# Kernel tuning notes

Measured on AMD Instinct MI355X. Metric: run time of the kernel, lower is better.

Reference implementation:

```python
import jax, jax.numpy as jnp
import numpy as np

B, C, T = 8, 1024, 1024
H, K, R = 8, 8, 8
DQK = C // K      # 128, per-head q/k channels
DFC1 = C // R     # 128, FC hidden
DINNER = C // H   # 128, per-head FC output


def setup_inputs() -> dict:
    key = jax.random.key(0)
    ks = jax.random.split(key, 12)
    s_in = 1.0 / np.sqrt(C)
    s_fc = 1.0 / np.sqrt(DFC1)
    return {
        "x": jax.random.normal(ks[0], (B, C, T), dtype=jnp.float32),
        # per-head 1x1 conv weights stacked over heads
        "Wq": jax.random.normal(ks[1], (H, DQK, C), dtype=jnp.float32) * s_in,
        "bq": jax.random.normal(ks[2], (H, DQK), dtype=jnp.float32) * 0.01,
        "Wk": jax.random.normal(ks[3], (H, DQK, C), dtype=jnp.float32) * s_in,
        "bk": jax.random.normal(ks[4], (H, DQK), dtype=jnp.float32) * 0.01,
        "Wv": jax.random.normal(ks[5], (H, C, C), dtype=jnp.float32) * s_in,
        "bv": jax.random.normal(ks[6], (H, C), dtype=jnp.float32) * 0.01,
        # gamma is zero-init in torch; use small random values to exercise the math
        "gamma": jax.random.normal(ks[7], (H,), dtype=jnp.float32) * 0.1,
        # post-concat MLP (nn.Linear weights, shape (out, in))
        "W1": jax.random.normal(ks[8], (DFC1, C), dtype=jnp.float32) * s_in,
        "b1": jax.random.normal(ks[9], (DFC1,), dtype=jnp.float32) * 0.01,
        "W2": jax.random.normal(ks[10], (DINNER, DFC1), dtype=jnp.float32) * s_fc,
        "b2": jax.random.normal(ks[11], (DINNER,), dtype=jnp.float32) * 0.01,
    }


def reference(x, Wq, bq, Wk, bk, Wv, bv, gamma, W1, b1, W2, b2):
    # x: (B, C, T). 1x1 Conv1d == channel-wise linear; batch all H heads at once.
    q = jnp.einsum('hoc,bct->bhot', Wq, x) + bq[None, :, :, None]  # (B,H,DQK,T)
    k = jnp.einsum('hoc,bct->bhot', Wk, x) + bk[None, :, :, None]  # (B,H,DQK,T)
    v = jnp.einsum('hoc,bct->bhot', Wv, x) + bv[None, :, :, None]  # (B,H,C,T)
    # energy[b,h,t,s] = q[:, :, :, t] . k[:, :, :, s]; softmax over s (no scaling, as in source)
    attn = jax.nn.softmax(jnp.einsum('bhot,bhos->bhts', q, k), axis=-1)  # (B,H,T,T)
    # out[b,h,c,t] = sum_s v[b,h,c,s] * attn[b,h,t,s]
    o = jnp.einsum('bhcs,bhts->bhct', v, attn)                     # (B,H,C,T)
    heads = gamma[None, :, None, None] * o + x[:, None, :, :]      # (B,H,C,T)
    # torch.stack(outs, 2): (B, C, H, T)
    out = heads.transpose(0, 2, 1, 3).reshape(B, C, H * T)
    out = out.transpose(0, 2, 1)                                   # (B, H*T, C)
    # fcs: Linear -> ReLU -> Dropout(eval: identity) -> Linear -> ReLU -> Dropout
    out = jax.nn.relu(out @ W1.T + b1)
    out = jax.nn.relu(out @ W2.T + b2)                             # (B, H*T, DINNER)
    out = out.transpose(0, 2, 1).reshape(B, DINNER * H, T)         # (B, C, T)
    return out + x
```

## Files before the change

kernel.cpp:

```cpp
#include <hip/hip_runtime.h>
#include <hip/hip_bf16.h>

typedef __hip_bfloat16 bf16;
typedef __attribute__((ext_vector_type(8))) __bf16 bf16x8;
typedef __attribute__((ext_vector_type(4))) float f32x4;

#define BM 128
#define BN 128

typedef const __attribute__((address_space(1))) void gvoid;
typedef __attribute__((address_space(3))) void lvoid;

template<int MODE>
__global__ __launch_bounds__(512)
void gemm256(const bf16* __restrict__ A, long lda, long sAb, long sAh,
             const bf16* __restrict__ B, long ldb, long sBb, long sBh,
             void* __restrict__ Cv, long ldc, long sCb, long sCh,
             int K,
             const float* __restrict__ bias, long sBiasZ,
             const float* __restrict__ gamma,
             const bf16* __restrict__ xt, long ldxt)
{
    __shared__ bf16 ring[3][(256 + 128) * 64];
    const int nt4 = blockIdx.x >> 3;
    const int zh  = blockIdx.x & 7;
    const int zb  = blockIdx.z;
    const bf16* Ab = A + (long)zb * sAb + (long)zh * sAh + (long)blockIdx.y * 256 * lda;
    const bf16* Bb = B + (long)zb * sBb + (long)zh * sBh + (long)nt4 * 128 * ldb;
    const int tid = threadIdx.x;
    const int wave = tid >> 6, lane = tid & 63;
    const int col = lane & 15, quad = lane >> 4;
    const int wm = (wave >> 1) * 64, wn = (wave & 1) * 64;

    const bf16* aAddr[4];
    const bf16* bAddr[2];
    int aDst[4], bDst[2];
    #pragma unroll
    for (int i = 0; i < 4; ++i) {
        int cbase = i * 512 + wave * 64;
        int c = cbase + lane;
        int m = c >> 3, j = c & 7;
        aAddr[i] = Ab + (long)m * lda + ((j ^ (m & 7)) << 3);
        aDst[i] = cbase * 8;
    }
    #pragma unroll
    for (int i = 0; i < 2; ++i) {
        int cbase = i * 512 + wave * 64;
        int c = cbase + lane;
        int m = c >> 3, j = c & 7;
        bAddr[i] = Bb + (long)m * ldb + ((j ^ (m & 7)) << 3);
        bDst[i] = 16384 + cbase * 8;
    }

    int offA[2][4], offB[2][4];
    #pragma unroll
    for (int x = 0; x < 2; ++x) {
        int kq = x * 4 + quad;
        #pragma unroll
        for (int mi = 0; mi < 4; ++mi) {
            int m = wm + mi * 16 + col;
            offA[x][mi] = m * 64 + ((kq ^ (m & 7)) << 3);
            int n = wn + mi * 16 + col;
            offB[x][mi] = 16384 + n * 64 + ((kq ^ (n & 7)) << 3);
        }
    }

    f32x4 acc[4][4] = {};

    auto STAGE = [&](int rb) {
        bf16* base = &ring[rb][0];
        #pragma unroll
        for (int i = 0; i < 4; ++i) {
            __builtin_amdgcn_global_load_lds((gvoid*)aAddr[i], (lvoid*)(base + aDst[i]), 16, 0, 0);
            aAddr[i] += 64;
        }
        #pragma unroll
        for (int i = 0; i < 2; ++i) {
            __builtin_amdgcn_global_load_lds((gvoid*)bAddr[i], (lvoid*)(base + bDst[i]), 16, 0, 0);
            bAddr[i] += 64;
        }
    };

    const int NT = K >> 6;
    STAGE(0);
    STAGE(1);
    asm volatile("s_waitcnt vmcnt(6)" ::: "memory");
    __builtin_amdgcn_s_barrier();
    __builtin_amdgcn_sched_barrier(0);

    int rc = 0;
    for (int t = 0; t < NT; ++t) {
        int r2 = rc + 2; if (r2 >= 3) r2 -= 3;
        if (t + 2 < NT) STAGE(r2);
        const bf16* buf = &ring[rc][0];
        #pragma unroll
        for (int x = 0; x < 2; ++x) {
            bf16x8 af[4], bfr[4];
            #pragma unroll
            for (int mi = 0; mi < 4; ++mi)
                af[mi] = *(const bf16x8*)(buf + offA[x][mi]);
            #pragma unroll
            for (int ni = 0; ni < 4; ++ni)
                bfr[ni] = *(const bf16x8*)(buf + offB[x][ni]);
            #pragma unroll
            for (int mi = 0; mi < 4; ++mi)
                #pragma unroll
                for (int ni = 0; ni < 4; ++ni)
                    acc[mi][ni] = __builtin_amdgcn_mfma_f32_16x16x32_bf16(
                        af[mi], bfr[ni], acc[mi][ni], 0, 0, 0);
        }
        if (t + 2 < NT)
            asm volatile("s_waitcnt vmcnt(6)" ::: "memory");
        else if (t + 1 < NT)
            asm volatile("s_waitcnt vmcnt(0)" ::: "memory");
        if (t + 1 < NT) {
            __builtin_amdgcn_s_barrier();
            __builtin_amdgcn_sched_barrier(0);
        }
        rc = rc + 1; if (rc >= 3) rc -= 3;
    }

    const long m0 = (long)blockIdx.y * 256 + wm;
    const long n0 = (long)nt4 * 128 + wn;
    float g = 0.f;
    if (MODE == 3) g = gamma[zh];
    #pragma unroll
    for (int mi = 0; mi < 4; ++mi) {
        #pragma unroll
        for (int ni = 0; ni < 4; ++ni) {
            long mb = m0 + mi * 16 + quad * 4;
            long n  = n0 + ni * 16 + col;
            if constexpr (MODE == 0) {
                bf16* cp = (bf16*)Cv + (long)zb * sCb + (long)zh * sCh + mb * ldc + n;
                const float* bp = bias + zh * sBiasZ + mb;
                #pragma unroll
                for (int r = 0; r < 4; ++r) {
                    *cp = __float2bfloat16(acc[mi][ni][r] + bp[r]);
                    cp += ldc;
                }
            } else {
                bf16* cp = (bf16*)Cv + (long)zb * sCb + (long)zh * sCh + mb * ldc + n;
                const bf16* xp = xt + (long)zb * 1048576 + mb * ldxt + n;
                #pragma unroll
                for (int r = 0; r < 4; ++r) {
                    float xv = __bfloat162float(*xp);
                    *cp = __float2bfloat16(g * acc[mi][ni][r] + xv);
                    cp += ldc;
                    xp += ldxt;
                }
            }
        }
    }
}

template<int MODE, int TBK, int LAYOUT>
__global__ __launch_bounds__(256)
void gemm_nt(const bf16* __restrict__ A, long lda, long sAb, long sAh,
             const bf16* __restrict__ B, long ldb, long sBb, long sBh,
             void* __restrict__ Cv, long ldc, long sCb, long sCh,
             int K,
             const float* __restrict__ bias, long sBiasZ,
             const float* __restrict__ gamma,
             const bf16* __restrict__ xt, long ldxt,
             const float* __restrict__ xf)
{
    __shared__ bf16 As[BM * TBK];
    __shared__ bf16 Bs[BN * TBK];
    const int bxt = (LAYOUT == 2) ? (blockIdx.x >> 3) : blockIdx.x;
    const int zb  = (LAYOUT == 2) ? blockIdx.z : (blockIdx.z >> 3);
    const int zh  = (LAYOUT == 2) ? (blockIdx.x & 7) : (blockIdx.z & 7);
    const bf16* Ab = A + (long)zb * sAb + (long)zh * sAh + (long)blockIdx.y * BM * lda;
    const bf16* Bb = B + (long)zb * sBb + (long)zh * sBh + (long)bxt * BN * ldb;
    const int tid  = threadIdx.x;
    const int wave = tid >> 6, lane = tid & 63;
    const int col  = lane & 15, quad = lane >> 4;
    const int wm = (wave & 1) * 64, wn = (wave >> 1) * 64;
    constexpr int CPR = TBK / 8;
    constexpr int NSLOT = TBK / 16;
    constexpr int NX = TBK / 32;

    const bf16* aAddr[NSLOT];
    const bf16* bAddr[NSLOT];
    #pragma unroll
    for (int i = 0; i < NSLOT; ++i) {
        int cbase = i * 256 + wave * 64;
        int c = cbase + lane;
        int m = c / CPR;
        int j = c % CPR;
        int kch = ((j ^ (m & 7)) << 3);
        aAddr[i] = Ab + (long)m * lda + kch;
        bAddr[i] = Bb + (long)m * ldb + kch;
    }

    int offA[NX][4], offB[NX][4];
    #pragma unroll
    for (int x = 0; x < NX; ++x) {
        int kq = x * 4 + quad;
        #pragma unroll
        for (int mi = 0; mi < 4; ++mi) {
            int m = wm + mi * 16 + col;
            offA[x][mi] = m * TBK + ((kq ^ (m & 7)) << 3);
            int n = wn + mi * 16 + col;
            offB[x][mi] = n * TBK + ((kq ^ (n & 7)) << 3);
        }
    }

    f32x4 acc[4][4] = {};

    for (int k0 = 0; k0 < K; k0 += TBK) {
        __syncthreads();
        #pragma unroll
        for (int i = 0; i < NSLOT; ++i) {
            int cbase = i * 256 + wave * 64;
            __builtin_amdgcn_global_load_lds(
                (gvoid*)aAddr[i], (lvoid*)(As + cbase * 8), 16, 0, 0);
            __builtin_amdgcn_global_load_lds(
                (gvoid*)bAddr[i], (lvoid*)(Bs + cbase * 8), 16, 0, 0);
            aAddr[i] += TBK;
            bAddr[i] += TBK;
        }
        __syncthreads();
        #pragma unroll
        for (int x = 0; x < NX; ++x) {
            bf16x8 af[4], bfr[4];
            #pragma unroll
            for (int mi = 0; mi < 4; ++mi)
                af[mi] = *(const bf16x8*)(As + offA[x][mi]);
            #pragma unroll
            for (int ni = 0; ni < 4; ++ni)
                bfr[ni] = *(const bf16x8*)(Bs + offB[x][ni]);
            #pragma unroll
            for (int mi = 0; mi < 4; ++mi)
                #pragma unroll
                for (int ni = 0; ni < 4; ++ni)
                    acc[mi][ni] = __builtin_amdgcn_mfma_f32_16x16x32_bf16(
                        af[mi], bfr[ni], acc[mi][ni], 0, 0, 0);
        }
    }

    const long m0 = (long)blockIdx.y * BM + wm;
    const long n0 = (long)bxt * BN + wn;
    float g = 0.f;
    if (MODE == 3) g = gamma[zh];

    float bn[4];
    if constexpr (MODE == 1 || MODE == 4 || MODE == 5) {
        #pragma unroll
        for (int ni = 0; ni < 4; ++ni)
            bn[ni] = bias[n0 + ni * 16 + col];
    }

    #pragma unroll
    for (int mi = 0; mi < 4; ++mi) {
        #pragma unroll
        for (int ni = 0; ni < 4; ++ni) {
            long mb = m0 + mi * 16 + quad * 4;
            long n  = n0 + ni * 16 + col;
            if constexpr (MODE == 0) {
                bf16* cp = (bf16*)Cv + (long)zb * sCb + (long)zh * sCh + mb * ldc + n;
                const float* bp = bias + zh * sBiasZ + mb;
                #pragma unroll
                for (int r = 0; r < 4; ++r) {
                    float v = acc[mi][ni][r] + bp[r];
                    *cp = __float2bfloat16(v);
                    cp += ldc;
                }
            } else if constexpr (MODE == 1) {
                bf16* cp = (bf16*)Cv + mb * ldc + n;
                #pragma unroll
                for (int r = 0; r < 4; ++r) {
                    float v = acc[mi][ni][r] + bn[ni];
                    *cp = __float2bfloat16(v);
                    cp += ldc;
                }
            } else if constexpr (MODE == 3) {
                bf16* cp = (bf16*)Cv + (long)zb * sCb + (long)zh * sCh + mb * ldc + n;
                const bf16* xp = xt + (long)zb * 1048576 + mb * ldxt + n;
                #pragma unroll
                for (int r = 0; r < 4; ++r) {
                    float xv = __bfloat162float(*xp);
                    *cp = __float2bfloat16(g * acc[mi][ni][r] + xv);
                    cp += ldc;
                    xp += ldxt;
                }
            } else if constexpr (MODE == 4) {
                bf16* cp = (bf16*)Cv + mb * ldc + n;
                #pragma unroll
                for (int r = 0; r < 4; ++r) {
                    float v = acc[mi][ni][r] + bn[ni];
                    v = v > 0.f ? v : 0.f;
                    *cp = __float2bfloat16(v);
                    cp += ldc;
                }
            } else {
                #pragma unroll
                for (int r = 0; r < 4; ++r) {
                    long m = mb + r;
                    float v = acc[mi][ni][r] + bn[ni];
                    v = v > 0.f ? v : 0.f;
                    long bb = m >> 13, h = (m >> 10) & 7, t = m & 1023;
                    long oi = bb * 1048576 + (n * 8 + h) * 1024 + t;
                    ((float*)Cv)[oi] = v + xf[oi];
                }
            }
        }
    }
}

__global__ __launch_bounds__(256, 2)
void attn_fused(const bf16* __restrict__ qk, bf16* __restrict__ attn)
{
    constexpr int PAD = 1032;
    __shared__ __align__(16) char smraw[40960];
    __shared__ float red[2][4][32];
    bf16* Qs = (bf16*)smraw;
    bf16* Ks = (bf16*)(smraw + 8192);
    bf16* Sbuf = (bf16*)smraw;

    const int z = blockIdx.x;
    const int zb = z >> 3, zh = z & 7;
    const int t0 = blockIdx.y * 32;
    const int tid = threadIdx.x, w = tid >> 6, lane = tid & 63;
    const int col = lane & 15, quad = lane >> 4;

    const bf16* Qbase = qk + ((long)zb * 1024 + t0) * 2048 + zh * 256;
    const bf16* Kbase = qk + (long)zb * 1024 * 2048 + zh * 256 + 128;

    #pragma unroll
    for (int i = 0; i < 2; ++i) {
        int cbase = i * 256 + w * 64;
        int c = cbase + lane;
        int m = c >> 4, j = c & 15;
        __builtin_amdgcn_global_load_lds(
            (gvoid*)(Qbase + (long)m * 2048 + ((j ^ (m & 7)) << 3)),
            (lvoid*)(Qs + cbase * 8), 16, 0, 0);
    }
    __syncthreads();
    bf16x8 af[2][4];
    #pragma unroll
    for (int mi = 0; mi < 2; ++mi) {
        int m = mi * 16 + col;
        #pragma unroll
        for (int ki = 0; ki < 4; ++ki)
            af[mi][ki] = *(const bf16x8*)(Qs + m * 128 + ((((ki << 2) + quad) ^ (m & 7)) << 3));
    }

    f32x4 acc[2][16] = {};
    #pragma unroll
    for (int si = 0; si < 8; ++si) {
        __syncthreads();
        const bf16* Kb = Kbase + (long)si * 128 * 2048;
        #pragma unroll
        for (int i = 0; i < 8; ++i) {
            int cbase = i * 256 + w * 64;
            int c = cbase + lane;
            int m = c >> 4, j = c & 15;
            __builtin_amdgcn_global_load_lds(
                (gvoid*)(Kb + (long)m * 2048 + ((j ^ (m & 7)) << 3)),
                (lvoid*)(Ks + cbase * 8), 16, 0, 0);
        }
        __syncthreads();
        bf16x8 bfr[2][4];
        #pragma unroll
        for (int ni = 0; ni < 2; ++ni) {
            int n = w * 32 + ni * 16 + col;
            #pragma unroll
            for (int ki = 0; ki < 4; ++ki)
                bfr[ni][ki] = *(const bf16x8*)(Ks + n * 128 + ((((ki << 2) + quad) ^ (n & 7)) << 3));
        }
        #pragma unroll
        for (int ki = 0; ki < 4; ++ki)
            #pragma unroll
            for (int mi = 0; mi < 2; ++mi)
                #pragma unroll
                for (int ni = 0; ni < 2; ++ni)
                    acc[mi][si * 2 + ni] = __builtin_amdgcn_mfma_f32_16x16x32_bf16(
                        af[mi][ki], bfr[ni][ki], acc[mi][si * 2 + ni], 0, 0, 0);
    }

    float rmx[2][4], rinv[2][4];
    #pragma unroll
    for (int mi = 0; mi < 2; ++mi)
        #pragma unroll
        for (int r = 0; r < 4; ++r) {
            float mx = acc[mi][0][r];
            #pragma unroll
            for (int j = 1; j < 16; ++j) mx = fmaxf(mx, acc[mi][j][r]);
            #pragma unroll
            for (int off = 1; off < 16; off <<= 1) mx = fmaxf(mx, __shfl_xor(mx, off, 64));
            rmx[mi][r] = mx;
        }
    if (col == 0) {
        #pragma unroll
        for (int mi = 0; mi < 2; ++mi)
            #pragma unroll
            for (int r = 0; r < 4; ++r)
                red[0][w][mi * 16 + quad * 4 + r] = rmx[mi][r];
    }
    __syncthreads();
    #pragma unroll
    for (int mi = 0; mi < 2; ++mi)
        #pragma unroll
        for (int r = 0; r < 4; ++r) {
            int row = mi * 16 + quad * 4 + r;
            rmx[mi][r] = fmaxf(fmaxf(red[0][0][row], red[0][1][row]),
                               fmaxf(red[0][2][row], red[0][3][row]));
        }
    #pragma unroll
    for (int mi = 0; mi < 2; ++mi)
        #pragma unroll
        for (int r = 0; r < 4; ++r) {
            float s = 0.f;
            #pragma unroll
            for (int j = 0; j < 16; ++j) {
                acc[mi][j][r] = __expf(acc[mi][j][r] - rmx[mi][r]);
                s += acc[mi][j][r];
            }
            #pragma unroll
            for (int off = 1; off < 16; off <<= 1) s += __shfl_xor(s, off, 64);
            rinv[mi][r] = s;
        }
    if (col == 0) {
        #pragma unroll
        for (int mi = 0; mi < 2; ++mi)
            #pragma unroll
            for (int r = 0; r < 4; ++r)
                red[1][w][mi * 16 + quad * 4 + r] = rinv[mi][r];
    }
    __syncthreads();
    #pragma unroll
    for (int mi = 0; mi < 2; ++mi)
        #pragma unroll
        for (int r = 0; r < 4; ++r) {
            int row = mi * 16 + quad * 4 + r;
            float s4 = red[1][0][row] + red[1][1][row] + red[1][2][row] + red[1][3][row];
            rinv[mi][r] = 1.0f / s4;
        }

    bf16* dst = attn + ((long)(zb * 8 + zh)) * 1048576 + (long)t0 * 1024;
    #pragma unroll
    for (int mi = 0; mi < 2; ++mi) {
        __syncthreads();
        #pragma unroll
        for (int j = 0; j < 16; ++j) {
            int colb = (j >> 1) * 128 + w * 32 + (j & 1) * 16 + col;
            #pragma unroll
            for (int r = 0; r < 4; ++r) {
                int rowh = quad * 4 + r;
                Sbuf[rowh * PAD + colb] = __float2bfloat16(acc[mi][j][r] * rinv[mi][r]);
            }
        }
        __syncthreads();
        #pragma unroll
        for (int i = 0; i < 8; ++i) {
            int c = i * 256 + tid;
            int rowh = c >> 7, jj = c & 127;
            bf16x8 vv = *(const bf16x8*)(Sbuf + rowh * PAD + jj * 8);
            *(bf16x8*)(dst + (long)(mi * 16 + rowh) * 1024 + jj * 8) = vv;
        }
    }
}

__global__ __launch_bounds__(256)
void transpose_cast_x(const float* __restrict__ x, bf16* __restrict__ xt)
{
    __shared__ float tile[32][33];
    int b = blockIdx.z;
    int c0 = blockIdx.y * 32, t0 = blockIdx.x * 32;
    int tx = threadIdx.x & 31, ty = threadIdx.x >> 5;
    const float* xb = x + (long)b * 1024 * 1024;
    #pragma unroll
    for (int i = 0; i < 4; ++i) {
        int c = ty + i * 8;
        tile[c][tx] = xb[(long)(c0 + c) * 1024 + t0 + tx];
    }
    __syncthreads();
    bf16* xtb = xt + (long)b * 1024 * 1024;
    #pragma unroll
    for (int i = 0; i < 4; ++i) {
        int t = ty + i * 8;
        xtb[(long)(t0 + t) * 1024 + c0 + tx] = __float2bfloat16(tile[tx][t]);
    }
}

__global__ __launch_bounds__(256)
void cast_f2b(const float* __restrict__ in, bf16* __restrict__ out, long n)
{
    long i = (long)blockIdx.x * 256 + threadIdx.x;
    long stride = (long)gridDim.x * 256;
    for (; i < n; i += stride) out[i] = __float2bfloat16(in[i]);
}

__global__ __launch_bounds__(256)
void build_wqk(const float* __restrict__ Wq, const float* __restrict__ Wk,
               const float* __restrict__ bq, const float* __restrict__ bk,
               bf16* __restrict__ Wqk, float* __restrict__ biasqk)
{
    long i = (long)blockIdx.x * 256 + threadIdx.x;
    long r = i >> 10, c = i & 1023;
    long h = r >> 8, rr = r & 255;
    float v = (rr < 128) ? Wq[(h * 128 + rr) * 1024 + c]
                         : Wk[(h * 128 + (rr - 128)) * 1024 + c];
    Wqk[i] = __float2bfloat16(v);
    if (c == 0)
        biasqk[r] = (rr < 128) ? bq[h * 128 + rr] : bk[h * 128 + rr - 128];
}

extern "C" void kernel_launch(void* const* d_in, const int* in_sizes, int n_in,
                              void* d_out, int out_size, void* d_ws, size_t ws_size,
                              hipStream_t stream)
{
    const float* x     = (const float*)d_in[0];
    const float* Wq    = (const float*)d_in[1];
    const float* bq    = (const float*)d_in[2];
    const float* Wk    = (const float*)d_in[3];
    const float* bk    = (const float*)d_in[4];
    const float* Wv    = (const float*)d_in[5];
    const float* bv    = (const float*)d_in[6];
    const float* gamma = (const float*)d_in[7];
    const float* W1    = (const float*)d_in[8];
    const float* b1    = (const float*)d_in[9];
    const float* W2    = (const float*)d_in[10];
    const float* b2    = (const float*)d_in[11];
    float* out = (float*)d_out;

    char* base = (char*)d_ws;
    const long MB = 1048576;
    bf16*  xt   = (bf16*)(base);
    bf16*  Wvb  = (bf16*)(base + 16 * MB);
    bf16*  vbuf = (bf16*)(base + 32 * MB);
    bf16*  Wqk  = (bf16*)(base + 32 * MB);
    float* bqk  = (float*)(base + 36 * MB);
    bf16*  attb = (bf16*)(base + 96 * MB);
    bf16*  W1b  = (bf16*)(base + 96 * MB);
    bf16*  W2b  = (bf16*)(base + 96 * MB + 524288);
    bf16*  y1c  = (bf16*)(base + 97 * MB);
    bf16*  ot   = (bf16*)(base + 160 * MB);
    bf16*  qkt  = (bf16*)(base + 224 * MB);

    dim3 blk(256);
    transpose_cast_x<<<dim3(32, 32, 8), blk, 0, stream>>>(x, xt);
    build_wqk<<<8192, blk, 0, stream>>>(Wq, Wk, bq, bk, Wqk, bqk);
    cast_f2b<<<4096, blk, 0, stream>>>(Wv, Wvb, 8192ll * 1024);

    const long M1 = 1048576, M2 = 2097152, M8 = 8388608;

    gemm_nt<1, 64, 0><<<dim3(16, 64, 1), blk, 0, stream>>>(
        xt, 1024, 0, 0, Wqk, 1024, 0, 0, qkt, 2048, 0, 0, 1024,
        bqk, 0, nullptr, nullptr, 0, nullptr);

    for (int q = 0; q < 2; ++q) {
        const long b0 = (long)q * 4;
        const bf16* xtq = xt + b0 * M1;
        gemm256<0><<<dim3(64, 4, 4), dim3(512), 0, stream>>>(
            Wvb, 1024, 0, M1, xtq, 1024, M1, 0, vbuf, 1024, M8, M1, 1024,
            bv, 1024, nullptr, nullptr, 0);
        attn_fused<<<dim3(32, 32, 1), blk, 0, stream>>>(
            qkt + b0 * M2, attb);
        gemm256<3><<<dim3(64, 4, 4), dim3(512), 0, stream>>>(
            attb, 1024, M8, M1, vbuf, 1024, M8, M1,
            ot, 1024, M8, M1, 1024,
            nullptr, 0, gamma, xtq, 1024);
        cast_f2b<<<512, blk, 0, stream>>>(W1, W1b, 128 * 1024);
        cast_f2b<<<64, blk, 0, stream>>>(W2, W2b, 128 * 128);
        gemm_nt<4, 64, 0><<<dim3(1, 256, 1), blk, 0, stream>>>(
            ot, 1024, 0, 0, W1b, 1024, 0, 0, y1c, 128, 0, 0, 1024,
            b1, 0, nullptr, nullptr, 0, nullptr);
        gemm_nt<5, 128, 0><<<dim3(1, 256, 1), blk, 0, stream>>>(
            y1c, 128, 0, 0, W2b, 128, 0, 0, out + b0 * M1, 0, 0, 0, 128,
            b2, 0, nullptr, nullptr, 0, x + b0 * M1);
    }
}
```

Before: 676.7 us.

## Halve gemm256 K-tile to 32 for occupancy, reuse it for QK projection

```diff
diff --git a/kernel.cpp b/kernel.cpp
--- a/kernel.cpp
+++ b/kernel.cpp
@@ -11,8 +11,8 @@
 typedef const __attribute__((address_space(1))) void gvoid;
 typedef __attribute__((address_space(3))) void lvoid;
 
-template<int MODE>
-__global__ __launch_bounds__(512)
+template<int MODE, int QKLAY>
+__global__ __launch_bounds__(512, 4)
 void gemm256(const bf16* __restrict__ A, long lda, long sAb, long sAh,
              const bf16* __restrict__ B, long ldb, long sBb, long sBh,
              void* __restrict__ Cv, long ldc, long sCb, long sCh,
@@ -21,10 +21,10 @@
              const float* __restrict__ gamma,
              const bf16* __restrict__ xt, long ldxt)
 {
-    __shared__ bf16 ring[3][(256 + 128) * 64];
-    const int nt4 = blockIdx.x >> 3;
-    const int zh  = blockIdx.x & 7;
-    const int zb  = blockIdx.z;
+    __shared__ bf16 ring[3][(256 + 128) * 32];
+    const int nt4 = QKLAY ? blockIdx.x : (blockIdx.x >> 3);
+    const int zh  = QKLAY ? 0 : (blockIdx.x & 7);
+    const int zb  = QKLAY ? 0 : blockIdx.z;
     const bf16* Ab = A + (long)zb * sAb + (long)zh * sAh + (long)blockIdx.y * 256 * lda;
     const bf16* Bb = B + (long)zb * sBb + (long)zh * sBh + (long)nt4 * 128 * ldb;
     const int tid = threadIdx.x;
@@ -32,37 +32,42 @@
     const int col = lane & 15, quad = lane >> 4;
     const int wm = (wave >> 1) * 64, wn = (wave & 1) * 64;
 
-    const bf16* aAddr[4];
-    const bf16* bAddr[2];
-    int aDst[4], bDst[2];
-    #pragma unroll
-    for (int i = 0; i < 4; ++i) {
-        int cbase = i * 512 + wave * 64;
-        int c = cbase + lane;
-        int m = c >> 3, j = c & 7;
-        aAddr[i] = Ab + (long)m * lda + ((j ^ (m & 7)) << 3);
-        aDst[i] = cbase * 8;
-    }
+    const bf16* aAddr[2];
+    const bf16* bAddr1;
+    int aDst[2], bDst1;
     #pragma unroll
     for (int i = 0; i < 2; ++i) {
         int cbase = i * 512 + wave * 64;
         int c = cbase + lane;
-        int m = c >> 3, j = c & 7;
-        bAddr[i] = Bb + (long)m * ldb + ((j ^ (m & 7)) << 3);
-        bDst[i] = 16384 + cbase * 8;
-    }
-
-    int offA[2][4], offB[2][4];
-    #pragma unroll
-    for (int x = 0; x < 2; ++x) {
-        int kq = x * 4 + quad;
-        #pragma unroll
-        for (int mi = 0; mi < 4; ++mi) {
-            int m = wm + mi * 16 + col;
-            offA[x][mi] = m * 64 + ((kq ^ (m & 7)) << 3);
-            int n = wn + mi * 16 + col;
-            offB[x][mi] = 16384 + n * 64 + ((kq ^ (n & 7)) << 3);
-        }
+        int p = c >> 3, s = c & 7;
+        int sp = s ^ (p & 7);
+        int m = 2 * p + (sp >> 2);
+        int j = sp & 3;
+        aAddr[i] = Ab + (long)m * lda + (j << 3);
+        aDst[i] = cbase * 8;
+    }
+    {
+        int cbase = wave * 64;
+        int c = cbase + lane;
+        int p = c >> 3, s = c & 7;
+        int sp = s ^ (p & 7);
+        int m = 2 * p + (sp >> 2);
+        int j = sp & 3;
+        bAddr1 = Bb + (long)m * ldb + (j << 3);
+        bDst1 = 8192 + cbase * 8;
+    }
+
+    int offA[4], offB[4];
+    #pragma unroll
+    for (int mi = 0; mi < 4; ++mi) {
+        int m = wm + mi * 16 + col;
+        int p = m >> 1;
+        int s = (quad | ((m & 1) << 2)) ^ (p & 7);
+        offA[mi] = p * 64 + s * 8;
+        int n = wn + mi * 16 + col;
+        int pn = n >> 1;
+        int sn = (quad | ((n & 1) << 2)) ^ (pn & 7);
+        offB[mi] = 8192 + pn * 64 + sn * 8;
     }
 
     f32x4 acc[4][4] = {};
@@ -70,21 +75,18 @@
     auto STAGE = [&](int rb) {
         bf16* base = &ring[rb][0];
         #pragma unroll
-        for (int i = 0; i < 4; ++i) {
+        for (int i = 0; i < 2; ++i) {
             __builtin_amdgcn_global_load_lds((gvoid*)aAddr[i], (lvoid*)(base + aDst[i]), 16, 0, 0);
-            aAddr[i] += 64;
-        }
-        #pragma unroll
-        for (int i = 0; i < 2; ++i) {
-            __builtin_amdgcn_global_load_lds((gvoid*)bAddr[i], (lvoid*)(base + bDst[i]), 16, 0, 0);
-            bAddr[i] += 64;
-        }
+            aAddr[i] += 32;
+        }
+        __builtin_amdgcn_global_load_lds((gvoid*)bAddr1, (lvoid*)(base + bDst1), 16, 0, 0);
+        bAddr1 += 32;
     };
 
-    const int NT = K >> 6;
+    const int NT = K >> 5;
     STAGE(0);
     STAGE(1);
-    asm volatile("s_waitcnt vmcnt(6)" ::: "memory");
+    asm volatile("s_waitcnt vmcnt(3)" ::: "memory");
     __builtin_amdgcn_s_barrier();
     __builtin_amdgcn_sched_barrier(0);
 
@@ -93,24 +95,21 @@
         int r2 = rc + 2; if (r2 >= 3) r2 -= 3;
         if (t + 2 < NT) STAGE(r2);
         const bf16* buf = &ring[rc][0];
-        #pragma unroll
-        for (int x = 0; x < 2; ++x) {
-            bf16x8 af[4], bfr[4];
-            #pragma unroll
-            for (int mi = 0; mi < 4; ++mi)
-                af[mi] = *(const bf16x8*)(buf + offA[x][mi]);
+        bf16x8 af[4], bfr[4];
+        #pragma unroll
+        for (int mi = 0; mi < 4; ++mi)
+            af[mi] = *(const bf16x8*)(buf + offA[mi]);
+        #pragma unroll
+        for (int ni = 0; ni < 4; ++ni)
+            bfr[ni] = *(const bf16x8*)(buf + offB[ni]);
+        #pragma unroll
+        for (int mi = 0; mi < 4; ++mi)
             #pragma unroll
             for (int ni = 0; ni < 4; ++ni)
-                bfr[ni] = *(const bf16x8*)(buf + offB[x][ni]);
-            #pragma unroll
-            for (int mi = 0; mi < 4; ++mi)
-                #pragma unroll
-                for (int ni = 0; ni < 4; ++ni)
-                    acc[mi][ni] = __builtin_amdgcn_mfma_f32_16x16x32_bf16(
-                        af[mi], bfr[ni], acc[mi][ni], 0, 0, 0);
-        }
+                acc[mi][ni] = __builtin_amdgcn_mfma_f32_16x16x32_bf16(
+                    af[mi], bfr[ni], acc[mi][ni], 0, 0, 0);
         if (t + 2 < NT)
-            asm volatile("s_waitcnt vmcnt(6)" ::: "memory");
+            asm volatile("s_waitcnt vmcnt(3)" ::: "memory");
         else if (t + 1 < NT)
             asm volatile("s_waitcnt vmcnt(0)" ::: "memory");
         if (t + 1 < NT) {
@@ -124,6 +123,12 @@
     const long n0 = (long)nt4 * 128 + wn;
     float g = 0.f;
     if (MODE == 3) g = gamma[zh];
+    float bn[4];
+    if constexpr (MODE == 1) {
+        #pragma unroll
+        for (int ni = 0; ni < 4; ++ni)
+            bn[ni] = bias[n0 + ni * 16 + col];
+    }
     #pragma unroll
     for (int mi = 0; mi < 4; ++mi) {
         #pragma unroll
@@ -136,6 +141,13 @@
                 #pragma unroll
                 for (int r = 0; r < 4; ++r) {
                     *cp = __float2bfloat16(acc[mi][ni][r] + bp[r]);
+                    cp += ldc;
+                }
+            } else if constexpr (MODE == 1) {
+                bf16* cp = (bf16*)Cv + mb * ldc + n;
+                #pragma unroll
+                for (int r = 0; r < 4; ++r) {
+                    *cp = __float2bfloat16(acc[mi][ni][r] + bn[ni]);
                     cp += ldc;
                 }
             } else {
@@ -545,19 +557,19 @@
 
     const long M1 = 1048576, M2 = 2097152, M8 = 8388608;
 
-    gemm_nt<1, 64, 0><<<dim3(16, 64, 1), blk, 0, stream>>>(
+    gemm256<1, 1><<<dim3(16, 32, 1), dim3(512), 0, stream>>>(
         xt, 1024, 0, 0, Wqk, 1024, 0, 0, qkt, 2048, 0, 0, 1024,
-        bqk, 0, nullptr, nullptr, 0, nullptr);
+        bqk, 0, nullptr, nullptr, 0);
 
     for (int q = 0; q < 2; ++q) {
         const long b0 = (long)q * 4;
         const bf16* xtq = xt + b0 * M1;
-        gemm256<0><<<dim3(64, 4, 4), dim3(512), 0, stream>>>(
+        gemm256<0, 0><<<dim3(64, 4, 4), dim3(512), 0, stream>>>(
             Wvb, 1024, 0, M1, xtq, 1024, M1, 0, vbuf, 1024, M8, M1, 1024,
             bv, 1024, nullptr, nullptr, 0);
         attn_fused<<<dim3(32, 32, 1), blk, 0, stream>>>(
             qkt + b0 * M2, attb);
-        gemm256<3><<<dim3(64, 4, 4), dim3(512), 0, stream>>>(
+        gemm256<3, 0><<<dim3(64, 4, 4), dim3(512), 0, stream>>>(
             attb, 1024, M8, M1, vbuf, 1024, M8, M1,
             ot, 1024, M8, M1, 1024,
             nullptr, 0, gamma, xtq, 1024);
```

After: 652.3 us. 3.6% less time.
